# Kernel optimization log

Hardware: AMD Instinct MI355X
Metric: run time of the kernel (lower is better)

The kernel has to match this reference:

```python
import jax, jax.numpy as jnp
import numpy as np

D_MODEL = 512
NHEAD = 8
HEAD_DIM = D_MODEL // NHEAD
LN_EPS = 1e-5


def layer_norm(x, gamma, beta):
    mu = jnp.mean(x, axis=-1, keepdims=True)
    var = jnp.var(x, axis=-1, keepdims=True)
    return (x - mu) * jax.lax.rsqrt(var + LN_EPS) * gamma + beta


def setup_inputs() -> dict:
    key = jax.random.key(0)
    ks = jax.random.split(key, 10)
    B, L, S = 2, 4096, 4096
    d = D_MODEL
    s = 0.02
    return {
        "x": jax.random.normal(ks[0], (B, L, d), dtype=jnp.float32),
        "source": jax.random.normal(ks[1], (B, S, d), dtype=jnp.float32),
        "Wq": jax.random.normal(ks[2], (d, d), dtype=jnp.float32) * s,
        "Wk": jax.random.normal(ks[3], (d, d), dtype=jnp.float32) * s,
        "Wv": jax.random.normal(ks[4], (d, d), dtype=jnp.float32) * s,
        "Wm": jax.random.normal(ks[5], (d, d), dtype=jnp.float32) * s,
        "W1": jax.random.normal(ks[6], (2 * d, 2 * d), dtype=jnp.float32) * s,
        "W2": jax.random.normal(ks[7], (d, 2 * d), dtype=jnp.float32) * s,
        "g1": jnp.ones((d,), dtype=jnp.float32),
        "b1": jnp.zeros((d,), dtype=jnp.float32),
        "g2": jnp.ones((d,), dtype=jnp.float32),
        "b2": jnp.zeros((d,), dtype=jnp.float32),
    }


def reference(x, source, Wq, Wk, Wv, Wm, W1, W2, g1, b1, g2, b2):
    bs, L, _ = x.shape
    S = source.shape[1]
    # projections (torch Linear: y = x @ W^T), split into heads
    qw = (x @ Wq.T).reshape(bs, L, NHEAD, HEAD_DIM)
    kw = (source @ Wk.T).reshape(bs, S, NHEAD, HEAD_DIM)
    vw = (source @ Wv.T).reshape(bs, S, NHEAD, HEAD_DIM)
    # attention scores [B, L, S, H], softmax over S (axis=2)
    a = jnp.einsum('nlhd,nshd->nlsh', qw, kw) / jnp.sqrt(jnp.float32(HEAD_DIM))
    a = jax.nn.softmax(a, axis=2)
    o = jnp.einsum('nlsh,nshd->nlhd', a, vw).reshape(bs, L, NHEAD * HEAD_DIM)
    message = layer_norm(o @ Wm.T, g1, b1)
    h = jnp.concatenate([x, message], axis=2)  # [B, L, 2D]
    h = jax.nn.relu(h @ W1.T) @ W2.T
    message = layer_norm(h, g2, b2)
    return x + message
```

## Files before the change

kernel.cpp:

```cpp
#include <hip/hip_runtime.h>
#include <stdint.h>

typedef short bh8 __attribute__((ext_vector_type(8)));
typedef float fx4 __attribute__((ext_vector_type(4)));
typedef float fx16 __attribute__((ext_vector_type(16)));
typedef unsigned short u16;
typedef unsigned int u32;
typedef u32 u32x4 __attribute__((ext_vector_type(4)));
typedef u16 us4 __attribute__((ext_vector_type(4)));

#define NHEAD 8
#define HD 64
#define DM 512
#define SEQ 4096
#define ROWS 8192
#define CEXP 0.1803368801111244f

#define MODE_BF16 1
#define MODE_RELU_BF16 2
#define MODE_KV 3

__device__ __forceinline__ u16 f2bf(float f) {
  union { float f; u32 u; } x; x.f = f;
  u32 u = x.u;
  u = u + 0x7fffu + ((u >> 16) & 1u);
  return (u16)(u >> 16);
}
__device__ __forceinline__ float bf2f(u16 h) {
  union { u32 u; float f; } x; x.u = ((u32)h) << 16;
  return x.f;
}
__device__ __forceinline__ void gll16(const void* g, void* l) {
  __builtin_amdgcn_global_load_lds(
      (const __attribute__((address_space(1))) void*)(uintptr_t)g,
      (__attribute__((address_space(3))) void*)(uintptr_t)l,
      16, 0, 0);
}
__device__ __forceinline__ fx4 mfma16(bh8 a, bh8 b, fx4 c) {
  return __builtin_amdgcn_mfma_f32_16x16x32_bf16(a, b, c, 0, 0, 0);
}
__device__ __forceinline__ fx16 mfma32(bh8 a, bh8 b, fx16 c) {
  return __builtin_amdgcn_mfma_f32_32x32x16_bf16(a, b, c, 0, 0, 0);
}
__device__ __forceinline__ u32 cvtpk(float lo, float hi) {
  u32 r; asm("v_cvt_pk_bf16_f32 %0, %1, %2" : "=v"(r) : "v"(lo), "v"(hi));
  return r;
}
__device__ __forceinline__ void pswap(u32& a, u32& b) {
  auto r = __builtin_amdgcn_permlane32_swap(a, b, false, false);
  a = r[0]; b = r[1];
}

__device__ __forceinline__ int fragidx4(int n, int k4, int K) {
  return (((((n >> 4) * (K >> 5) + (k4 >> 5)) << 2) + ((k4 >> 3) & 3)) * 16 + (n & 15)) * 2
         + ((k4 & 7) >> 2);
}

__global__ __launch_bounds__(256) void cvt_all_kernel(
    const float* __restrict__ x, const float* __restrict__ src,
    const float* __restrict__ Wq, const float* __restrict__ Wk,
    const float* __restrict__ Wv, const float* __restrict__ Wm,
    const float* __restrict__ W1, const float* __restrict__ W2,
    u16* __restrict__ xb, u16* __restrict__ sb,
    u16* __restrict__ wqb, u16* __restrict__ wkvb, u16* __restrict__ wmb,
    u16* __restrict__ w1b, u16* __restrict__ w2b) {
  const int NQ = ROWS * DM / 4;
  const int TOT = 2 * NQ + 655360;
  for (int i = blockIdx.x * 256 + threadIdx.x; i < TOT; i += gridDim.x * 256) {
    const float* s; u16* d; int j; int widx = -1;
    if (i < NQ)            { s = x;  d = xb;  j = i; }
    else if (i < 2 * NQ)   { s = src; d = sb; j = i - NQ; }
    else {
      int k = i - 2 * NQ;
      int n, k4, K;
      if (k < 65536)       { s = Wq; d = wqb; j = k;          n = j >> 7; k4 = (j & 127) << 2; K = 512; }
      else if (k < 131072) { s = Wk; d = wkvb; j = k - 65536; n = j >> 7; k4 = (j & 127) << 2; K = 512; }
      else if (k < 196608) { s = Wv; d = wkvb; j = k - 131072; n = (j >> 7) + 512; k4 = (j & 127) << 2; K = 512; }
      else if (k < 262144) { s = Wm; d = wmb; j = k - 196608; n = j >> 7; k4 = (j & 127) << 2; K = 512; }
      else if (k < 524288) { s = W1; d = w1b; j = k - 262144; n = j >> 8; k4 = (j & 255) << 2; K = 1024; }
      else                 { s = W2; d = w2b; j = k - 524288; n = j >> 8; k4 = (j & 255) << 2; K = 1024; }
      widx = fragidx4(n, k4, K);
    }
    float4 v = ((const float4*)s)[j];
    us4 o; o.x = f2bf(v.x); o.y = f2bf(v.y); o.z = f2bf(v.z); o.w = f2bf(v.w);
    ((us4*)d)[widx < 0 ? j : widx] = o;
  }
}

template <int NTW>
__device__ __forceinline__ void gemm_core(
    char* smem, const u16* __restrict__ A, const u16* __restrict__ A2, int strideA,
    const u16* __restrict__ Bw, void* __restrict__ Cp, void* __restrict__ C2p,
    int N, int K, int mode, float scl, int bx, int by) {
  const int tid = threadIdx.x;
  const int w = tid >> 6, l = tid & 63;
  const int fr = l & 15, fg = l >> 4;
  const int row0 = by * 128, col0 = bx * NTW * 32;
  const int wr = (w >> 1) * 64, wc = (w & 1) * NTW * 16;

  auto STAGE = [&](int buf, int k0) {
    const u16* Asrc = (k0 < 512) ? A : A2;
    const int kk = k0 & (strideA - 1);
    char* dst = smem + buf * 16384;
#pragma unroll
    for (int i = 0; i < 4; i++) {
      int t = i * 256 + tid;
      int rr = t >> 3, g = t & 7;
      int gs = g ^ (rr & 7);
      gll16(Asrc + (size_t)(row0 + rr) * strideA + kk + gs * 8, dst + i * 4096 + w * 1024);
    }
  };

  fx4 acc[4][NTW];
#pragma unroll
  for (int m = 0; m < 4; m++)
#pragma unroll
    for (int n = 0; n < NTW; n++)
#pragma unroll
      for (int r = 0; r < 4; r++) acc[m][n][r] = 0.f;

  STAGE(0, 0);
  __syncthreads();

  const int nk = K / 64;
  for (int ti = 0; ti < nk; ti++) {
    const int k0 = ti * 64;
    bh8 bfr[2][NTW];
#pragma unroll
    for (int ks = 0; ks < 2; ks++)
#pragma unroll
      for (int n = 0; n < NTW; n++) {
        const u16* bp = Bw +
            ((((size_t)((col0 + wc) >> 4) + n) * (K >> 5) + (k0 >> 5) + ks) * 4 + fg) * 128 +
            fr * 8;
        bfr[ks][n] = *(const bh8*)bp;
      }
    if (ti + 1 < nk) STAGE((ti + 1) & 1, k0 + 64);
    const char* sA = smem + (ti & 1) * 16384;
#pragma unroll
    for (int ks = 0; ks < 2; ks++) {
      bh8 af[4];
#pragma unroll
      for (int m = 0; m < 4; m++) {
        int rr = wr + m * 16 + fr;
        af[m] = *(const bh8*)(sA + rr * 128 + ((ks * 64 + fg * 16) ^ ((rr & 7) << 4)));
      }
      __builtin_amdgcn_s_setprio(1);
#pragma unroll
      for (int m = 0; m < 4; m++)
#pragma unroll
        for (int n = 0; n < NTW; n++) acc[m][n] = mfma16(af[m], bfr[ks][n], acc[m][n]);
      __builtin_amdgcn_s_setprio(0);
    }
    __syncthreads();
  }
#pragma unroll
  for (int m = 0; m < 4; m++)
#pragma unroll
    for (int n = 0; n < NTW; n++)
#pragma unroll
      for (int r = 0; r < 4; r++) {
        int row = row0 + wr + m * 16 + fg * 4 + r;
        int col = col0 + wc + n * 16 + fr;
        float v = acc[m][n][r];
        if (mode == MODE_BF16) {
          ((u16*)Cp)[(size_t)row * N + col] = f2bf(v * scl);
        } else if (mode == MODE_RELU_BF16) {
          ((u16*)Cp)[(size_t)row * N + col] = f2bf(v > 0.f ? v : 0.f);
        } else {
          int bb = row >> 12, s = row & 4095;
          if (col < 512) {
            int h = col >> 6, dd = col & 63;
            ((u16*)Cp)[(((size_t)((bb * 8 + h) * 8 + (dd >> 3))) * SEQ + s) * 8 + (dd & 7)] = f2bf(v);
          } else {
            int dd2 = col - 512;
            int h = dd2 >> 6, dd = dd2 & 63;
            ((u16*)C2p)[(((size_t)((bb * 8 + h) * 512 + (s >> 3))) * 64 + dd) * 8 + (s & 7)] = f2bf(v);
          }
        }
      }
}

__global__ __launch_bounds__(256) void qkv_kernel(
    const u16* __restrict__ xb, const u16* __restrict__ sb,
    const u16* __restrict__ wqb, const u16* __restrict__ wkvb,
    u16* __restrict__ Qb, u16* __restrict__ K2, u16* __restrict__ V2) {
  __shared__ __attribute__((aligned(16))) char smem[2 * 16384];
  int bid = blockIdx.x;
  if (bid < 256) {
    gemm_core<4>(smem, xb, xb, 512, wqb, Qb, nullptr, 512, 512, MODE_BF16, CEXP,
                 bid & 3, bid >> 2);
  } else {
    int kb = bid - 256;
    gemm_core<4>(smem, sb, sb, 512, wkvb, K2, V2, 1024, 512, MODE_KV, 1.0f,
                 kb & 7, kb >> 3);
  }
}

__global__ __launch_bounds__(256) void ffn1_kernel(
    const u16* __restrict__ xb, const u16* __restrict__ m0ln,
    const u16* __restrict__ w1b, u16* __restrict__ h1) {
  __shared__ __attribute__((aligned(16))) char smem[2 * 16384];
  gemm_core<4>(smem, xb, m0ln, 512, w1b, h1, nullptr, 1024, 1024, MODE_RELU_BF16, 1.0f,
               blockIdx.x, blockIdx.y);
}

__global__ __launch_bounds__(256) void gemm64_kernel(
    const u16* __restrict__ A, const u16* __restrict__ A2, int strideA,
    const u16* __restrict__ Bw, u16* __restrict__ Cp, int K, float scl) {
  __shared__ __attribute__((aligned(16))) char smem[2 * 16384];
  gemm_core<2>(smem, A, A2, strideA, Bw, Cp, nullptr, 512, K, MODE_BF16, scl,
               blockIdx.x, blockIdx.y);
}

__global__ __launch_bounds__(256, 3) void attn_kernel(
    const u16* __restrict__ Q, const u16* __restrict__ K2,
    const u16* __restrict__ V2,
    u16* __restrict__ Op0, u16* __restrict__ Op1,
    u16* __restrict__ Op2, u16* __restrict__ Op3,
    float* __restrict__ lsum, int ss) {
  const int tid = threadIdx.x;
  const int w = tid >> 6, l = tid & 63;
  const int l31 = l & 31, hi = l >> 5;

  int dl = blockIdx.x;
  int c = dl & 7, j = dl >> 3;
  int bh = 2 * c + (j >> (5 + ss));
  int rest = j & ((32 << ss) - 1);
  int qb = rest & 31, half = rest >> 5;
  const int b = bh >> 3, h = bh & 7;
  const int qr0 = b * SEQ + qb * 128 + w * 32;
  const int chunk = SEQ >> ss;
  const int sbase = half * chunk;
  const int NT = chunk / 64;

  bh8 qf[4];
#pragma unroll
  for (int ks = 0; ks < 4; ks++)
    qf[ks] = *(const bh8*)(Q + (size_t)(qr0 + l31) * DM + h * HD + ks * 16 + hi * 8);

  const u16* Kbase = K2 + (size_t)bh * 8 * SEQ * 8;
  const u16* Vbase = V2 + (size_t)bh * 512 * 64 * 8;

  const u16* kp[4]; const u16* vp[4];
#pragma unroll
  for (int ks = 0; ks < 4; ks++) {
    kp[ks] = Kbase + ((size_t)(ks * 2 + hi) * SEQ + sbase + l31) * 8;
    vp[ks] = Vbase + ((size_t)(((sbase >> 3) + ks * 2 + hi)) * 64 + l31) * 8;
  }

  fx16 o0, o1;
#pragma unroll
  for (int r = 0; r < 16; r++) { o0[r] = 0.f; o1[r] = 0.f; }
  float l_run = 0.f;

  for (int t = 0; t < NT; ++t) {
    bh8 kf0[4], kf1[4];
#pragma unroll
    for (int ks = 0; ks < 4; ks++) {
      kf0[ks] = *(const bh8*)kp[ks];
      kf1[ks] = *(const bh8*)(kp[ks] + 256);
    }

    fx16 s0v, s1v;
#pragma unroll
    for (int r = 0; r < 16; r++) { s0v[r] = 0.f; s1v[r] = 0.f; }
    __builtin_amdgcn_s_setprio(1);
#pragma unroll
    for (int ks = 0; ks < 4; ks++) {
      s0v = mfma32(kf0[ks], qf[ks], s0v);
      s1v = mfma32(kf1[ks], qf[ks], s1v);
    }
    __builtin_amdgcn_s_setprio(0);

    bh8 vf0[4], vf1[4];
#pragma unroll
    for (int ks = 0; ks < 4; ks++) {
      vf0[ks] = *(const bh8*)vp[ks];
      vf1[ks] = *(const bh8*)(vp[ks] + 256);
    }
#pragma unroll
    for (int ks = 0; ks < 4; ks++) { kp[ks] += 512; vp[ks] += 4096; }

    float rs = 0.f;
#pragma unroll
    for (int r = 0; r < 16; r++) {
      s0v[r] = __builtin_amdgcn_exp2f(s0v[r]); rs += s0v[r];
    }
#pragma unroll
    for (int r = 0; r < 16; r++) {
      s1v[r] = __builtin_amdgcn_exp2f(s1v[r]); rs += s1v[r];
    }
    l_run += rs;

    __builtin_amdgcn_s_setprio(1);
#pragma unroll
    for (int ks = 0; ks < 4; ks++) {
      int o8 = (ks & 1) * 8;
      u32 w0a, w1a, w0b, w1b;
      if (ks < 2) {
        w0a = cvtpk(s0v[o8 + 0], s0v[o8 + 1]);
        w1a = cvtpk(s0v[o8 + 2], s0v[o8 + 3]);
        w0b = cvtpk(s0v[o8 + 4], s0v[o8 + 5]);
        w1b = cvtpk(s0v[o8 + 6], s0v[o8 + 7]);
      } else {
        w0a = cvtpk(s1v[o8 + 0], s1v[o8 + 1]);
        w1a = cvtpk(s1v[o8 + 2], s1v[o8 + 3]);
        w0b = cvtpk(s1v[o8 + 4], s1v[o8 + 5]);
        w1b = cvtpk(s1v[o8 + 6], s1v[o8 + 7]);
      }
      pswap(w0a, w0b); pswap(w1a, w1b);
      u32x4 fw; fw.x = w0a; fw.y = w1a; fw.z = w0b; fw.w = w1b;
      bh8 pa = __builtin_bit_cast(bh8, fw);
      o0 = mfma32(pa, vf0[ks], o0);
      o1 = mfma32(pa, vf1[ks], o1);
    }
    __builtin_amdgcn_s_setprio(0);
  }

  l_run += __shfl_xor(l_run, 32);
  if (hi == 0)
    lsum[half * 65536 + bh * 4096 + ((qr0 & 4095) + l31)] = l_run;
  u16* Op = (half == 0) ? Op0 : (half == 1) ? Op1 : (half == 2) ? Op2 : Op3;
#pragma unroll
  for (int r = 0; r < 16; r++) {
    int crow = (r & 3) + 8 * (r >> 2) + 4 * hi;
    size_t row = (size_t)(qr0 + crow);
    Op[row * DM + h * HD + l31] = f2bf(o0[r]);
    Op[row * DM + h * HD + 32 + l31] = f2bf(o1[r]);
  }
}

__global__ __launch_bounds__(256) void merge_kernel(
    const u16* __restrict__ Oa, const u16* __restrict__ Ob,
    const u16* __restrict__ Oc, const u16* __restrict__ Od,
    const float* __restrict__ lsum, u16* __restrict__ out, int split) {
  int i8 = blockIdx.x * 256 + threadIdx.x;
  size_t base = (size_t)i8 * 8;
  if (base >= (size_t)ROWS * DM) return;
  int row = (int)(base >> 9), col = (int)(base & 511);
  int h = col >> 6, b = row >> 12, lr = row & 4095;
  int li = (b * 8 + h) * 4096 + lr;
  float acc[8];
#pragma unroll
  for (int j = 0; j < 8; j++) acc[j] = 0.f;
  float lt = 0.f;
  const u16* ops[4] = {Oa, Ob, Oc, Od};
  for (int s = 0; s < split; s++) {
    lt += lsum[s * 65536 + li];
    bh8 v = *(const bh8*)(ops[s] + base);
#pragma unroll
    for (int j = 0; j < 8; j++) acc[j] += bf2f((u16)v[j]);
  }
  float inv = 1.f / lt;
  bh8 o;
#pragma unroll
  for (int j = 0; j < 8; j++) o[j] = (short)f2bf(acc[j] * inv);
  *(bh8*)(out + base) = o;
}

__global__ __launch_bounds__(256) void ln_kernel(
    const u16* __restrict__ M0, const float* __restrict__ g1,
    const float* __restrict__ b1, u16* __restrict__ out) {
  const int row = blockIdx.x;
  const int tid = threadIdx.x;
  const u16* mr = M0 + (size_t)row * 512;
  float v0 = bf2f(mr[tid]), v1 = bf2f(mr[tid + 256]);
  float s = v0 + v1, s2 = v0 * v0 + v1 * v1;
#pragma unroll
  for (int off = 1; off <= 32; off <<= 1) {
    s += __shfl_xor(s, off);
    s2 += __shfl_xor(s2, off);
  }
  __shared__ float red[8];
  const int w = tid >> 6, l = tid & 63;
  if (l == 0) { red[w] = s; red[w + 4] = s2; }
  __syncthreads();
  s = red[0] + red[1] + red[2] + red[3];
  s2 = red[4] + red[5] + red[6] + red[7];
  float mu = s * (1.f / 512.f);
  float var = s2 * (1.f / 512.f) - mu * mu;
  float rstd = rsqrtf(var + 1e-5f);
  u16* orow = out + (size_t)row * 512;
  for (int e = tid; e < 512; e += 256)
    orow[e] = f2bf((bf2f(mr[e]) - mu) * rstd * g1[e] + b1[e]);
}

__global__ __launch_bounds__(256) void ln_res_kernel(
    const u16* __restrict__ F, const float* __restrict__ X,
    const float* __restrict__ g2, const float* __restrict__ b2,
    float* __restrict__ out) {
  const int row = blockIdx.x;
  const int tid = threadIdx.x;
  const u16* fr_ = F + (size_t)row * 512;
  float v0 = bf2f(fr_[tid]), v1 = bf2f(fr_[tid + 256]);
  float s = v0 + v1, s2 = v0 * v0 + v1 * v1;
#pragma unroll
  for (int off = 1; off <= 32; off <<= 1) {
    s += __shfl_xor(s, off);
    s2 += __shfl_xor(s2, off);
  }
  __shared__ float red[8];
  const int w = tid >> 6, l = tid & 63;
  if (l == 0) { red[w] = s; red[w + 4] = s2; }
  __syncthreads();
  s = red[0] + red[1] + red[2] + red[3];
  s2 = red[4] + red[5] + red[6] + red[7];
  float mu = s * (1.f / 512.f);
  float var = s2 * (1.f / 512.f) - mu * mu;
  float rstd = rsqrtf(var + 1e-5f);
  const float* xr = X + (size_t)row * 512;
  float* orow = out + (size_t)row * 512;
  for (int e = tid; e < 512; e += 256)
    orow[e] = xr[e] + (bf2f(fr_[e]) - mu) * rstd * g2[e] + b2[e];
}

extern "C" void kernel_launch(void* const* d_in, const int* in_sizes, int n_in,
                              void* d_out, int out_size, void* d_ws, size_t ws_size,
                              hipStream_t stream) {
  (void)in_sizes; (void)n_in; (void)out_size; (void)ws_size;
  const float* x   = (const float*)d_in[0];
  const float* src = (const float*)d_in[1];
  const float* Wq  = (const float*)d_in[2];
  const float* Wk  = (const float*)d_in[3];
  const float* Wv  = (const float*)d_in[4];
  const float* Wm  = (const float*)d_in[5];
  const float* W1  = (const float*)d_in[6];
  const float* W2  = (const float*)d_in[7];
  const float* g1  = (const float*)d_in[8];
  const float* b1  = (const float*)d_in[9];
  const float* g2  = (const float*)d_in[10];
  const float* b2  = (const float*)d_in[11];

  char* ws = (char*)d_ws;
  u16* xb   = (u16*)(ws + 0);
  u16* sb   = (u16*)(ws + 8388608);
  u16* wqb  = (u16*)(ws + 16777216);
  u16* wkvb = (u16*)(ws + 17301504);
  u16* wmb  = (u16*)(ws + 18350080);
  u16* w1b  = (u16*)(ws + 18874368);
  u16* w2b  = (u16*)(ws + 20971520);
  u16* Qb   = (u16*)(ws + 22020096);
  u16* K2b  = (u16*)(ws + 30408704);
  u16* V2b  = (u16*)(ws + 38797312);
  u16* Op0  = (u16*)(ws + 47185920);
  u16* Op1  = (u16*)(ws + 8388608);
  float* lsum = (float*)(ws + 55574528);

  const int ss = 1;
  u16* Obf  = (u16*)(ws + 22020096);
  u16* M0b  = (u16*)(ws + 30408704);
  u16* m0ln = (u16*)(ws + 38797312);
  u16* h1b  = (u16*)(ws + 22020096);
  u16* fb   = (u16*)(ws + 47185920);

  cvt_all_kernel<<<2048, 256, 0, stream>>>(x, src, Wq, Wk, Wv, Wm, W1, W2,
                                           xb, sb, wqb, wkvb, wmb, w1b, w2b);
  qkv_kernel<<<768, 256, 0, stream>>>(xb, sb, wqb, wkvb, Qb, K2b, V2b);
  attn_kernel<<<512 << ss, 256, 0, stream>>>(Qb, K2b, V2b, Op0, Op1, Op0, Op0, lsum, ss);
  merge_kernel<<<2048, 256, 0, stream>>>(Op0, Op1, Op0, Op0, lsum, Obf, 1 << ss);
  gemm64_kernel<<<dim3(8, 64), 256, 0, stream>>>(Obf, Obf, 512, wmb, M0b, 512, 1.0f);
  ln_kernel<<<8192, 256, 0, stream>>>(M0b, g1, b1, m0ln);
  ffn1_kernel<<<dim3(8, 64), 256, 0, stream>>>(xb, m0ln, w1b, h1b);
  gemm64_kernel<<<dim3(8, 64), 256, 0, stream>>>(h1b, h1b, 1024, w2b, fb, 1024, 1.0f);
  ln_res_kernel<<<8192, 256, 0, stream>>>(fb, x, g2, b2, (float*)d_out);
}
```

Measured before the change: 215.1 us.

## Store GEMM activations in MFMA fragment layout and drop LDS staging

All GEMM A-operands (x, source, attention output, layernorm output, ReLU hidden) are now written by their producer kernels directly in the MFMA fragment-tiled layout. The GEMM core can then load A fragments straight from global memory with 16-byte per-lane loads, like B, and drops the LDS double-buffered staging and per-tile barriers. The layernorm kernels are also reworked to one wavefront per row with 8-element vector loads and no shared-memory reduction. The trade-off is no LDS reuse of A across the waves that share rows, so each wave reads A from global/L2 on its own, and there is no explicit prefetch.

```diff
diff --git a/kernel.cpp b/kernel.cpp
--- a/kernel.cpp
+++ b/kernel.cpp
@@ -17,7 +17,7 @@
 #define CEXP 0.1803368801111244f
 
 #define MODE_BF16 1
-#define MODE_RELU_BF16 2
+#define MODE_RELU_FRAG 2
 #define MODE_KV 3
 
 __device__ __forceinline__ u16 f2bf(float f) {
@@ -29,12 +29,6 @@
 __device__ __forceinline__ float bf2f(u16 h) {
   union { u32 u; float f; } x; x.u = ((u32)h) << 16;
   return x.f;
-}
-__device__ __forceinline__ void gll16(const void* g, void* l) {
-  __builtin_amdgcn_global_load_lds(
-      (const __attribute__((address_space(1))) void*)(uintptr_t)g,
-      (__attribute__((address_space(3))) void*)(uintptr_t)l,
-      16, 0, 0);
 }
 __device__ __forceinline__ fx4 mfma16(bh8 a, bh8 b, fx4 c) {
   return __builtin_amdgcn_mfma_f32_16x16x32_bf16(a, b, c, 0, 0, 0);
@@ -67,29 +61,27 @@
   const int NQ = ROWS * DM / 4;
   const int TOT = 2 * NQ + 655360;
   for (int i = blockIdx.x * 256 + threadIdx.x; i < TOT; i += gridDim.x * 256) {
-    const float* s; u16* d; int j; int widx = -1;
-    if (i < NQ)            { s = x;  d = xb;  j = i; }
-    else if (i < 2 * NQ)   { s = src; d = sb; j = i - NQ; }
+    const float* s; u16* d; int j, n, k4, K;
+    if (i < NQ)            { s = x;  d = xb; j = i;      n = j >> 7; k4 = (j & 127) << 2; K = 512; }
+    else if (i < 2 * NQ)   { s = src; d = sb; j = i - NQ; n = j >> 7; k4 = (j & 127) << 2; K = 512; }
     else {
       int k = i - 2 * NQ;
-      int n, k4, K;
       if (k < 65536)       { s = Wq; d = wqb; j = k;          n = j >> 7; k4 = (j & 127) << 2; K = 512; }
       else if (k < 131072) { s = Wk; d = wkvb; j = k - 65536; n = j >> 7; k4 = (j & 127) << 2; K = 512; }
       else if (k < 196608) { s = Wv; d = wkvb; j = k - 131072; n = (j >> 7) + 512; k4 = (j & 127) << 2; K = 512; }
       else if (k < 262144) { s = Wm; d = wmb; j = k - 196608; n = j >> 7; k4 = (j & 127) << 2; K = 512; }
       else if (k < 524288) { s = W1; d = w1b; j = k - 262144; n = j >> 8; k4 = (j & 255) << 2; K = 1024; }
       else                 { s = W2; d = w2b; j = k - 524288; n = j >> 8; k4 = (j & 255) << 2; K = 1024; }
-      widx = fragidx4(n, k4, K);
     }
     float4 v = ((const float4*)s)[j];
     us4 o; o.x = f2bf(v.x); o.y = f2bf(v.y); o.z = f2bf(v.z); o.w = f2bf(v.w);
-    ((us4*)d)[widx < 0 ? j : widx] = o;
+    ((us4*)d)[fragidx4(n, k4, K)] = o;
   }
 }
 
 template <int NTW>
 __device__ __forceinline__ void gemm_core(
-    char* smem, const u16* __restrict__ A, const u16* __restrict__ A2, int strideA,
+    const u16* __restrict__ Af, int KA, const u16* __restrict__ Af2,
     const u16* __restrict__ Bw, void* __restrict__ Cp, void* __restrict__ C2p,
     int N, int K, int mode, float scl, int bx, int by) {
   const int tid = threadIdx.x;
@@ -98,18 +90,14 @@
   const int row0 = by * 128, col0 = bx * NTW * 32;
   const int wr = (w >> 1) * 64, wc = (w & 1) * NTW * 16;
 
-  auto STAGE = [&](int buf, int k0) {
-    const u16* Asrc = (k0 < 512) ? A : A2;
-    const int kk = k0 & (strideA - 1);
-    char* dst = smem + buf * 16384;
-#pragma unroll
-    for (int i = 0; i < 4; i++) {
-      int t = i * 256 + tid;
-      int rr = t >> 3, g = t & 7;
-      int gs = g ^ (rr & 7);
-      gll16(Asrc + (size_t)(row0 + rr) * strideA + kk + gs * 8, dst + i * 4096 + w * 1024);
-    }
-  };
+  const u16* ap[4];
+  const u16* bp[NTW];
+#pragma unroll
+  for (int m = 0; m < 4; m++)
+    ap[m] = Af + ((size_t)(((row0 + wr) >> 4) + m) * (KA >> 5)) * 512 + l * 8;
+#pragma unroll
+  for (int n = 0; n < NTW; n++)
+    bp[n] = Bw + ((size_t)(((col0 + wc) >> 4) + n) * (K >> 5)) * 512 + l * 8;
 
   fx4 acc[4][NTW];
 #pragma unroll
@@ -119,41 +107,39 @@
 #pragma unroll
       for (int r = 0; r < 4; r++) acc[m][n][r] = 0.f;
 
-  STAGE(0, 0);
-  __syncthreads();
-
-  const int nk = K / 64;
-  for (int ti = 0; ti < nk; ti++) {
-    const int k0 = ti * 64;
-    bh8 bfr[2][NTW];
-#pragma unroll
-    for (int ks = 0; ks < 2; ks++)
-#pragma unroll
-      for (int n = 0; n < NTW; n++) {
-        const u16* bp = Bw +
-            ((((size_t)((col0 + wc) >> 4) + n) * (K >> 5) + (k0 >> 5) + ks) * 4 + fg) * 128 +
-            fr * 8;
-        bfr[ks][n] = *(const bh8*)bp;
-      }
-    if (ti + 1 < nk) STAGE((ti + 1) & 1, k0 + 64);
-    const char* sA = smem + (ti & 1) * 16384;
-#pragma unroll
-    for (int ks = 0; ks < 2; ks++) {
-      bh8 af[4];
-#pragma unroll
-      for (int m = 0; m < 4; m++) {
-        int rr = wr + m * 16 + fr;
-        af[m] = *(const bh8*)(sA + rr * 128 + ((ks * 64 + fg * 16) ^ ((rr & 7) << 4)));
-      }
-      __builtin_amdgcn_s_setprio(1);
+  for (int k0 = 0; k0 < K; k0 += 64) {
+    if (K > 512 && KA == 512 && k0 == 512) {
 #pragma unroll
       for (int m = 0; m < 4; m++)
-#pragma unroll
-        for (int n = 0; n < NTW; n++) acc[m][n] = mfma16(af[m], bfr[ks][n], acc[m][n]);
-      __builtin_amdgcn_s_setprio(0);
-    }
-    __syncthreads();
-  }
+        ap[m] = Af2 + ((size_t)(((row0 + wr) >> 4) + m) * 16) * 512 + l * 8;
+    }
+    bh8 a0[4], a1[4], b0[NTW], b1[NTW];
+#pragma unroll
+    for (int m = 0; m < 4; m++) {
+      a0[m] = *(const bh8*)ap[m];
+      a1[m] = *(const bh8*)(ap[m] + 512);
+    }
+#pragma unroll
+    for (int n = 0; n < NTW; n++) {
+      b0[n] = *(const bh8*)bp[n];
+      b1[n] = *(const bh8*)(bp[n] + 512);
+    }
+#pragma unroll
+    for (int m = 0; m < 4; m++) ap[m] += 1024;
+#pragma unroll
+    for (int n = 0; n < NTW; n++) bp[n] += 1024;
+    __builtin_amdgcn_s_setprio(1);
+#pragma unroll
+    for (int m = 0; m < 4; m++)
+#pragma unroll
+      for (int n = 0; n < NTW; n++) acc[m][n] = mfma16(a0[m], b0[n], acc[m][n]);
+#pragma unroll
+    for (int m = 0; m < 4; m++)
+#pragma unroll
+      for (int n = 0; n < NTW; n++) acc[m][n] = mfma16(a1[m], b1[n], acc[m][n]);
+    __builtin_amdgcn_s_setprio(0);
+  }
+
 #pragma unroll
   for (int m = 0; m < 4; m++)
 #pragma unroll
@@ -165,8 +151,10 @@
         float v = acc[m][n][r];
         if (mode == MODE_BF16) {
           ((u16*)Cp)[(size_t)row * N + col] = f2bf(v * scl);
-        } else if (mode == MODE_RELU_BF16) {
-          ((u16*)Cp)[(size_t)row * N + col] = f2bf(v > 0.f ? v : 0.f);
+        } else if (mode == MODE_RELU_FRAG) {
+          int chunk = (row >> 4) * 32 + (col >> 5);
+          int lp = (row & 15) + ((col >> 3) & 3) * 16;
+          ((u16*)Cp)[((size_t)chunk * 64 + lp) * 8 + (col & 7)] = f2bf(v > 0.f ? v : 0.f);
         } else {
           int bb = row >> 12, s = row & 4095;
           if (col < 512) {
@@ -185,14 +173,13 @@
     const u16* __restrict__ xb, const u16* __restrict__ sb,
     const u16* __restrict__ wqb, const u16* __restrict__ wkvb,
     u16* __restrict__ Qb, u16* __restrict__ K2, u16* __restrict__ V2) {
-  __shared__ __attribute__((aligned(16))) char smem[2 * 16384];
   int bid = blockIdx.x;
   if (bid < 256) {
-    gemm_core<4>(smem, xb, xb, 512, wqb, Qb, nullptr, 512, 512, MODE_BF16, CEXP,
+    gemm_core<4>(xb, 512, xb, wqb, Qb, nullptr, 512, 512, MODE_BF16, CEXP,
                  bid & 3, bid >> 2);
   } else {
     int kb = bid - 256;
-    gemm_core<4>(smem, sb, sb, 512, wkvb, K2, V2, 1024, 512, MODE_KV, 1.0f,
+    gemm_core<4>(sb, 512, sb, wkvb, K2, V2, 1024, 512, MODE_KV, 1.0f,
                  kb & 7, kb >> 3);
   }
 }
@@ -200,16 +187,14 @@
 __global__ __launch_bounds__(256) void ffn1_kernel(
     const u16* __restrict__ xb, const u16* __restrict__ m0ln,
     const u16* __restrict__ w1b, u16* __restrict__ h1) {
-  __shared__ __attribute__((aligned(16))) char smem[2 * 16384];
-  gemm_core<4>(smem, xb, m0ln, 512, w1b, h1, nullptr, 1024, 1024, MODE_RELU_BF16, 1.0f,
+  gemm_core<4>(xb, 512, m0ln, w1b, h1, nullptr, 1024, 1024, MODE_RELU_FRAG, 1.0f,
                blockIdx.x, blockIdx.y);
 }
 
 __global__ __launch_bounds__(256) void gemm64_kernel(
-    const u16* __restrict__ A, const u16* __restrict__ A2, int strideA,
+    const u16* __restrict__ Af, int KA, const u16* __restrict__ Af2,
     const u16* __restrict__ Bw, u16* __restrict__ Cp, int K, float scl) {
-  __shared__ __attribute__((aligned(16))) char smem[2 * 16384];
-  gemm_core<2>(smem, A, A2, strideA, Bw, Cp, nullptr, 512, K, MODE_BF16, scl,
+  gemm_core<2>(Af, KA, Af2, Bw, Cp, nullptr, 512, K, MODE_BF16, scl,
                blockIdx.x, blockIdx.y);
 }
 
@@ -217,7 +202,6 @@
     const u16* __restrict__ Q, const u16* __restrict__ K2,
     const u16* __restrict__ V2,
     u16* __restrict__ Op0, u16* __restrict__ Op1,
-    u16* __restrict__ Op2, u16* __restrict__ Op3,
     float* __restrict__ lsum, int ss) {
   const int tid = threadIdx.x;
   const int w = tid >> 6, l = tid & 63;
@@ -321,7 +305,7 @@
   l_run += __shfl_xor(l_run, 32);
   if (hi == 0)
     lsum[half * 65536 + bh * 4096 + ((qr0 & 4095) + l31)] = l_run;
-  u16* Op = (half == 0) ? Op0 : (half == 1) ? Op1 : (half == 2) ? Op2 : Op3;
+  u16* Op = (half == 0) ? Op0 : Op1;
 #pragma unroll
   for (int r = 0; r < 16; r++) {
     int crow = (r & 3) + 8 * (r >> 2) + 4 * hi;
@@ -333,86 +317,77 @@
 
 __global__ __launch_bounds__(256) void merge_kernel(
     const u16* __restrict__ Oa, const u16* __restrict__ Ob,
-    const u16* __restrict__ Oc, const u16* __restrict__ Od,
-    const float* __restrict__ lsum, u16* __restrict__ out, int split) {
+    const float* __restrict__ lsum, u16* __restrict__ out) {
   int i8 = blockIdx.x * 256 + threadIdx.x;
   size_t base = (size_t)i8 * 8;
   if (base >= (size_t)ROWS * DM) return;
   int row = (int)(base >> 9), col = (int)(base & 511);
   int h = col >> 6, b = row >> 12, lr = row & 4095;
   int li = (b * 8 + h) * 4096 + lr;
-  float acc[8];
-#pragma unroll
-  for (int j = 0; j < 8; j++) acc[j] = 0.f;
-  float lt = 0.f;
-  const u16* ops[4] = {Oa, Ob, Oc, Od};
-  for (int s = 0; s < split; s++) {
-    lt += lsum[s * 65536 + li];
-    bh8 v = *(const bh8*)(ops[s] + base);
-#pragma unroll
-    for (int j = 0; j < 8; j++) acc[j] += bf2f((u16)v[j]);
-  }
-  float inv = 1.f / lt;
+  float la = lsum[li], lb = lsum[65536 + li];
+  float inv = 1.f / (la + lb);
+  bh8 va = *(const bh8*)(Oa + base);
+  bh8 vb = *(const bh8*)(Ob + base);
   bh8 o;
 #pragma unroll
-  for (int j = 0; j < 8; j++) o[j] = (short)f2bf(acc[j] * inv);
-  *(bh8*)(out + base) = o;
+  for (int j = 0; j < 8; j++)
+    o[j] = (short)f2bf((bf2f((u16)va[j]) + bf2f((u16)vb[j])) * inv);
+  int chunk = (row >> 4) * 16 + (col >> 5);
+  int lp = (row & 15) + ((col >> 3) & 3) * 16;
+  *(bh8*)(out + ((size_t)chunk * 64 + lp) * 8) = o;
 }
 
 __global__ __launch_bounds__(256) void ln_kernel(
     const u16* __restrict__ M0, const float* __restrict__ g1,
     const float* __restrict__ b1, u16* __restrict__ out) {
-  const int row = blockIdx.x;
-  const int tid = threadIdx.x;
-  const u16* mr = M0 + (size_t)row * 512;
-  float v0 = bf2f(mr[tid]), v1 = bf2f(mr[tid + 256]);
-  float s = v0 + v1, s2 = v0 * v0 + v1 * v1;
+  const int row = blockIdx.x * 4 + (threadIdx.x >> 6);
+  const int lane = threadIdx.x & 63;
+  bh8 v = *(const bh8*)(M0 + (size_t)row * 512 + lane * 8);
+  float f[8], s = 0.f, s2 = 0.f;
+#pragma unroll
+  for (int j = 0; j < 8; j++) { f[j] = bf2f((u16)v[j]); s += f[j]; s2 += f[j] * f[j]; }
 #pragma unroll
   for (int off = 1; off <= 32; off <<= 1) {
     s += __shfl_xor(s, off);
     s2 += __shfl_xor(s2, off);
   }
-  __shared__ float red[8];
-  const int w = tid >> 6, l = tid & 63;
-  if (l == 0) { red[w] = s; red[w + 4] = s2; }
-  __syncthreads();
-  s = red[0] + red[1] + red[2] + red[3];
-  s2 = red[4] + red[5] + red[6] + red[7];
   float mu = s * (1.f / 512.f);
   float var = s2 * (1.f / 512.f) - mu * mu;
   float rstd = rsqrtf(var + 1e-5f);
-  u16* orow = out + (size_t)row * 512;
-  for (int e = tid; e < 512; e += 256)
-    orow[e] = f2bf((bf2f(mr[e]) - mu) * rstd * g1[e] + b1[e]);
+  int col = lane * 8;
+  bh8 o;
+#pragma unroll
+  for (int j = 0; j < 8; j++)
+    o[j] = (short)f2bf((f[j] - mu) * rstd * g1[col + j] + b1[col + j]);
+  int chunk = (row >> 4) * 16 + (col >> 5);
+  int lp = (row & 15) + ((col >> 3) & 3) * 16;
+  *(bh8*)(out + ((size_t)chunk * 64 + lp) * 8) = o;
 }
 
 __global__ __launch_bounds__(256) void ln_res_kernel(
     const u16* __restrict__ F, const float* __restrict__ X,
     const float* __restrict__ g2, const float* __restrict__ b2,
     float* __restrict__ out) {
-  const int row = blockIdx.x;
-  const int tid = threadIdx.x;
-  const u16* fr_ = F + (size_t)row * 512;
-  float v0 = bf2f(fr_[tid]), v1 = bf2f(fr_[tid + 256]);
-  float s = v0 + v1, s2 = v0 * v0 + v1 * v1;
+  const int row = blockIdx.x * 4 + (threadIdx.x >> 6);
+  const int lane = threadIdx.x & 63;
+  bh8 v = *(const bh8*)(F + (size_t)row * 512 + lane * 8);
+  float f[8], s = 0.f, s2 = 0.f;
+#pragma unroll
+  for (int j = 0; j < 8; j++) { f[j] = bf2f((u16)v[j]); s += f[j]; s2 += f[j] * f[j]; }
 #pragma unroll
   for (int off = 1; off <= 32; off <<= 1) {
     s += __shfl_xor(s, off);
     s2 += __shfl_xor(s2, off);
   }
-  __shared__ float red[8];
-  const int w = tid >> 6, l = tid & 63;
-  if (l == 0) { red[w] = s; red[w + 4] = s2; }
-  __syncthreads();
-  s = red[0] + red[1] + red[2] + red[3];
-  s2 = red[4] + red[5] + red[6] + red[7];
   float mu = s * (1.f / 512.f);
   float var = s2 * (1.f / 512.f) - mu * mu;
   float rstd = rsqrtf(var + 1e-5f);
-  const float* xr = X + (size_t)row * 512;
-  float* orow = out + (size_t)row * 512;
-  for (int e = tid; e < 512; e += 256)
-    orow[e] = xr[e] + (bf2f(fr_[e]) - mu) * rstd * g2[e] + b2[e];
+  int col = lane * 8;
+  const float* xr = X + (size_t)row * 512 + col;
+  float* orow = out + (size_t)row * 512 + col;
+#pragma unroll
+  for (int j = 0; j < 8; j++)
+    orow[j] = xr[j] + (f[j] - mu) * rstd * g2[col + j] + b2[col + j];
 }
 
 extern "C" void kernel_launch(void* const* d_in, const int* in_sizes, int n_in,
@@ -457,11 +432,11 @@
   cvt_all_kernel<<<2048, 256, 0, stream>>>(x, src, Wq, Wk, Wv, Wm, W1, W2,
                                            xb, sb, wqb, wkvb, wmb, w1b, w2b);
   qkv_kernel<<<768, 256, 0, stream>>>(xb, sb, wqb, wkvb, Qb, K2b, V2b);
-  attn_kernel<<<512 << ss, 256, 0, stream>>>(Qb, K2b, V2b, Op0, Op1, Op0, Op0, lsum, ss);
-  merge_kernel<<<2048, 256, 0, stream>>>(Op0, Op1, Op0, Op0, lsum, Obf, 1 << ss);
-  gemm64_kernel<<<dim3(8, 64), 256, 0, stream>>>(Obf, Obf, 512, wmb, M0b, 512, 1.0f);
-  ln_kernel<<<8192, 256, 0, stream>>>(M0b, g1, b1, m0ln);
+  attn_kernel<<<512 << ss, 256, 0, stream>>>(Qb, K2b, V2b, Op0, Op1, lsum, ss);
+  merge_kernel<<<2048, 256, 0, stream>>>(Op0, Op1, lsum, Obf);
+  gemm64_kernel<<<dim3(8, 64), 256, 0, stream>>>(Obf, 512, Obf, wmb, M0b, 512, 1.0f);
+  ln_kernel<<<2048, 256, 0, stream>>>(M0b, g1, b1, m0ln);
   ffn1_kernel<<<dim3(8, 64), 256, 0, stream>>>(xb, m0ln, w1b, h1b);
-  gemm64_kernel<<<dim3(8, 64), 256, 0, stream>>>(h1b, h1b, 1024, w2b, fb, 1024, 1.0f);
-  ln_res_kernel<<<8192, 256, 0, stream>>>(fb, x, g2, b2, (float*)d_out);
-}
+  gemm64_kernel<<<dim3(8, 64), 256, 0, stream>>>(h1b, 1024, h1b, w2b, fb, 1024, 1.0f);
+  ln_res_kernel<<<2048, 256, 0, stream>>>(fb, x, g2, b2, (float*)d_out);
+}
```

New measurement: 218.0 us. About the same (+1.3%).

## Drop split-KV attention and merge pass; use one warp per row in LayerNorm

Applied to the files above, without the earlier changes.

Attention no longer splits the key sequence into two halves. Each block now covers the full 4096 keys and normalizes its output in-kernel using the lane-shuffled row sum, so the separate merge kernel and the partial-output and lsum buffers are gone. Both LayerNorm kernels now give each row to one 64-lane wave with 8-wide vector loads and stores, which removes the shared-memory reduction and __syncthreads. The trade-off is that the attention grid halves to 512 blocks, which may leave compute units underused on this GPU.

```diff
diff --git a/kernel.cpp b/kernel.cpp
--- a/kernel.cpp
+++ b/kernel.cpp
@@ -215,24 +215,18 @@
 
 __global__ __launch_bounds__(256, 3) void attn_kernel(
     const u16* __restrict__ Q, const u16* __restrict__ K2,
-    const u16* __restrict__ V2,
-    u16* __restrict__ Op0, u16* __restrict__ Op1,
-    u16* __restrict__ Op2, u16* __restrict__ Op3,
-    float* __restrict__ lsum, int ss) {
+    const u16* __restrict__ V2, u16* __restrict__ O) {
   const int tid = threadIdx.x;
   const int w = tid >> 6, l = tid & 63;
   const int l31 = l & 31, hi = l >> 5;
 
   int dl = blockIdx.x;
   int c = dl & 7, j = dl >> 3;
-  int bh = 2 * c + (j >> (5 + ss));
-  int rest = j & ((32 << ss) - 1);
-  int qb = rest & 31, half = rest >> 5;
+  int bh = 2 * c + (j >> 5);
+  int qb = j & 31;
   const int b = bh >> 3, h = bh & 7;
   const int qr0 = b * SEQ + qb * 128 + w * 32;
-  const int chunk = SEQ >> ss;
-  const int sbase = half * chunk;
-  const int NT = chunk / 64;
+  const int NT = SEQ / 64;
 
   bh8 qf[4];
 #pragma unroll
@@ -245,8 +239,8 @@
   const u16* kp[4]; const u16* vp[4];
 #pragma unroll
   for (int ks = 0; ks < 4; ks++) {
-    kp[ks] = Kbase + ((size_t)(ks * 2 + hi) * SEQ + sbase + l31) * 8;
-    vp[ks] = Vbase + ((size_t)(((sbase >> 3) + ks * 2 + hi)) * 64 + l31) * 8;
+    kp[ks] = Kbase + ((size_t)(ks * 2 + hi) * SEQ + l31) * 8;
+    vp[ks] = Vbase + ((size_t)(ks * 2 + hi) * 64 + l31) * 8;
   }
 
   fx16 o0, o1;
@@ -319,100 +313,65 @@
   }
 
   l_run += __shfl_xor(l_run, 32);
-  if (hi == 0)
-    lsum[half * 65536 + bh * 4096 + ((qr0 & 4095) + l31)] = l_run;
-  u16* Op = (half == 0) ? Op0 : (half == 1) ? Op1 : (half == 2) ? Op2 : Op3;
 #pragma unroll
   for (int r = 0; r < 16; r++) {
     int crow = (r & 3) + 8 * (r >> 2) + 4 * hi;
+    float li = 1.0f / __shfl(l_run, crow);
     size_t row = (size_t)(qr0 + crow);
-    Op[row * DM + h * HD + l31] = f2bf(o0[r]);
-    Op[row * DM + h * HD + 32 + l31] = f2bf(o1[r]);
-  }
-}
-
-__global__ __launch_bounds__(256) void merge_kernel(
-    const u16* __restrict__ Oa, const u16* __restrict__ Ob,
-    const u16* __restrict__ Oc, const u16* __restrict__ Od,
-    const float* __restrict__ lsum, u16* __restrict__ out, int split) {
-  int i8 = blockIdx.x * 256 + threadIdx.x;
-  size_t base = (size_t)i8 * 8;
-  if (base >= (size_t)ROWS * DM) return;
-  int row = (int)(base >> 9), col = (int)(base & 511);
-  int h = col >> 6, b = row >> 12, lr = row & 4095;
-  int li = (b * 8 + h) * 4096 + lr;
-  float acc[8];
-#pragma unroll
-  for (int j = 0; j < 8; j++) acc[j] = 0.f;
-  float lt = 0.f;
-  const u16* ops[4] = {Oa, Ob, Oc, Od};
-  for (int s = 0; s < split; s++) {
-    lt += lsum[s * 65536 + li];
-    bh8 v = *(const bh8*)(ops[s] + base);
-#pragma unroll
-    for (int j = 0; j < 8; j++) acc[j] += bf2f((u16)v[j]);
-  }
-  float inv = 1.f / lt;
-  bh8 o;
-#pragma unroll
-  for (int j = 0; j < 8; j++) o[j] = (short)f2bf(acc[j] * inv);
-  *(bh8*)(out + base) = o;
+    O[row * DM + h * HD + l31] = f2bf(o0[r] * li);
+    O[row * DM + h * HD + 32 + l31] = f2bf(o1[r] * li);
+  }
 }
 
 __global__ __launch_bounds__(256) void ln_kernel(
     const u16* __restrict__ M0, const float* __restrict__ g1,
     const float* __restrict__ b1, u16* __restrict__ out) {
-  const int row = blockIdx.x;
-  const int tid = threadIdx.x;
-  const u16* mr = M0 + (size_t)row * 512;
-  float v0 = bf2f(mr[tid]), v1 = bf2f(mr[tid + 256]);
-  float s = v0 + v1, s2 = v0 * v0 + v1 * v1;
+  const int row = blockIdx.x * 4 + (threadIdx.x >> 6);
+  const int lane = threadIdx.x & 63;
+  bh8 v = *(const bh8*)(M0 + (size_t)row * 512 + lane * 8);
+  float f[8], s = 0.f, s2 = 0.f;
+#pragma unroll
+  for (int j = 0; j < 8; j++) { f[j] = bf2f((u16)v[j]); s += f[j]; s2 += f[j] * f[j]; }
 #pragma unroll
   for (int off = 1; off <= 32; off <<= 1) {
     s += __shfl_xor(s, off);
     s2 += __shfl_xor(s2, off);
   }
-  __shared__ float red[8];
-  const int w = tid >> 6, l = tid & 63;
-  if (l == 0) { red[w] = s; red[w + 4] = s2; }
-  __syncthreads();
-  s = red[0] + red[1] + red[2] + red[3];
-  s2 = red[4] + red[5] + red[6] + red[7];
   float mu = s * (1.f / 512.f);
   float var = s2 * (1.f / 512.f) - mu * mu;
   float rstd = rsqrtf(var + 1e-5f);
-  u16* orow = out + (size_t)row * 512;
-  for (int e = tid; e < 512; e += 256)
-    orow[e] = f2bf((bf2f(mr[e]) - mu) * rstd * g1[e] + b1[e]);
+  int col = lane * 8;
+  bh8 o;
+#pragma unroll
+  for (int j = 0; j < 8; j++)
+    o[j] = (short)f2bf((f[j] - mu) * rstd * g1[col + j] + b1[col + j]);
+  *(bh8*)(out + (size_t)row * 512 + col) = o;
 }
 
 __global__ __launch_bounds__(256) void ln_res_kernel(
     const u16* __restrict__ F, const float* __restrict__ X,
     const float* __restrict__ g2, const float* __restrict__ b2,
     float* __restrict__ out) {
-  const int row = blockIdx.x;
-  const int tid = threadIdx.x;
-  const u16* fr_ = F + (size_t)row * 512;
-  float v0 = bf2f(fr_[tid]), v1 = bf2f(fr_[tid + 256]);
-  float s = v0 + v1, s2 = v0 * v0 + v1 * v1;
+  const int row = blockIdx.x * 4 + (threadIdx.x >> 6);
+  const int lane = threadIdx.x & 63;
+  bh8 v = *(const bh8*)(F + (size_t)row * 512 + lane * 8);
+  float f[8], s = 0.f, s2 = 0.f;
+#pragma unroll
+  for (int j = 0; j < 8; j++) { f[j] = bf2f((u16)v[j]); s += f[j]; s2 += f[j] * f[j]; }
 #pragma unroll
   for (int off = 1; off <= 32; off <<= 1) {
     s += __shfl_xor(s, off);
     s2 += __shfl_xor(s2, off);
   }
-  __shared__ float red[8];
-  const int w = tid >> 6, l = tid & 63;
-  if (l == 0) { red[w] = s; red[w + 4] = s2; }
-  __syncthreads();
-  s = red[0] + red[1] + red[2] + red[3];
-  s2 = red[4] + red[5] + red[6] + red[7];
   float mu = s * (1.f / 512.f);
   float var = s2 * (1.f / 512.f) - mu * mu;
   float rstd = rsqrtf(var + 1e-5f);
-  const float* xr = X + (size_t)row * 512;
-  float* orow = out + (size_t)row * 512;
-  for (int e = tid; e < 512; e += 256)
-    orow[e] = xr[e] + (bf2f(fr_[e]) - mu) * rstd * g2[e] + b2[e];
+  int col = lane * 8;
+  const float* xr = X + (size_t)row * 512 + col;
+  float* orow = out + (size_t)row * 512 + col;
+#pragma unroll
+  for (int j = 0; j < 8; j++)
+    orow[j] = xr[j] + (f[j] - mu) * rstd * g2[col + j] + b2[col + j];
 }
 
 extern "C" void kernel_launch(void* const* d_in, const int* in_sizes, int n_in,
@@ -443,25 +402,20 @@
   u16* Qb   = (u16*)(ws + 22020096);
   u16* K2b  = (u16*)(ws + 30408704);
   u16* V2b  = (u16*)(ws + 38797312);
-  u16* Op0  = (u16*)(ws + 47185920);
-  u16* Op1  = (u16*)(ws + 8388608);
-  float* lsum = (float*)(ws + 55574528);
-
-  const int ss = 1;
-  u16* Obf  = (u16*)(ws + 22020096);
+  u16* Ob   = (u16*)(ws + 47185920);
+
   u16* M0b  = (u16*)(ws + 30408704);
   u16* m0ln = (u16*)(ws + 38797312);
   u16* h1b  = (u16*)(ws + 22020096);
-  u16* fb   = (u16*)(ws + 47185920);
+  u16* fb   = (u16*)(ws + 8388608);
 
   cvt_all_kernel<<<2048, 256, 0, stream>>>(x, src, Wq, Wk, Wv, Wm, W1, W2,
                                            xb, sb, wqb, wkvb, wmb, w1b, w2b);
   qkv_kernel<<<768, 256, 0, stream>>>(xb, sb, wqb, wkvb, Qb, K2b, V2b);
-  attn_kernel<<<512 << ss, 256, 0, stream>>>(Qb, K2b, V2b, Op0, Op1, Op0, Op0, lsum, ss);
-  merge_kernel<<<2048, 256, 0, stream>>>(Op0, Op1, Op0, Op0, lsum, Obf, 1 << ss);
-  gemm64_kernel<<<dim3(8, 64), 256, 0, stream>>>(Obf, Obf, 512, wmb, M0b, 512, 1.0f);
-  ln_kernel<<<8192, 256, 0, stream>>>(M0b, g1, b1, m0ln);
+  attn_kernel<<<512, 256, 0, stream>>>(Qb, K2b, V2b, Ob);
+  gemm64_kernel<<<dim3(8, 64), 256, 0, stream>>>(Ob, Ob, 512, wmb, M0b, 512, 1.0f);
+  ln_kernel<<<2048, 256, 0, stream>>>(M0b, g1, b1, m0ln);
   ffn1_kernel<<<dim3(8, 64), 256, 0, stream>>>(xb, m0ln, w1b, h1b);
   gemm64_kernel<<<dim3(8, 64), 256, 0, stream>>>(h1b, h1b, 1024, w2b, fb, 1024, 1.0f);
-  ln_res_kernel<<<8192, 256, 0, stream>>>(fb, x, g2, b2, (float*)d_out);
-}
+  ln_res_kernel<<<2048, 256, 0, stream>>>(fb, x, g2, b2, (float*)d_out);
+}
```

Result: faster. 198.7 us (-7.7%).
